# Optimization experiments

Measured on AMD Instinct MI355X. Metric: run time of the kernel, lower is better.

The kernel has to match this reference:

```python
import jax, jax.numpy as jnp
import numpy as np

DIM = 768
D_STATE = 64
D_CONV = 4
EXPAND = 2
D_INNER = EXPAND * DIM          # 1536
DT_RANK = (DIM + 15) // 16      # 48
BATCH = 2
SEQ = 1024
EPS = 1e-5


def setup_inputs() -> dict:
    key = jax.random.key(0)
    ks = jax.random.split(key, 10)
    s = 0.02
    x = jax.random.normal(ks[0], (BATCH, SEQ, DIM), dtype=jnp.float32)
    gamma = jnp.ones((DIM,), jnp.float32)
    beta = jnp.zeros((DIM,), jnp.float32)
    W_in = jax.random.normal(ks[1], (2 * D_INNER, DIM), jnp.float32) * s
    conv_w = jax.random.normal(ks[2], (D_INNER, D_CONV), jnp.float32) * s
    conv_b = jnp.zeros((D_INNER,), jnp.float32)
    W_x = jax.random.normal(ks[3], (DT_RANK + 2 * D_STATE, D_INNER), jnp.float32) * s
    W_dt = jax.random.normal(ks[4], (D_INNER, DT_RANK), jnp.float32) * s
    b_dt = jax.random.uniform(ks[5], (D_INNER,), jnp.float32, -4.0, -2.0)  # dt bias ~ log-space init
    # S4D-real init: A_log[d, n] = log(n+1)
    A_log = jnp.log(jnp.broadcast_to(jnp.arange(1, D_STATE + 1, dtype=jnp.float32), (D_INNER, D_STATE)))
    D = jnp.ones((D_INNER,), jnp.float32)
    W_out = jax.random.normal(ks[6], (DIM, D_INNER), jnp.float32) * s
    return {"x": x, "gamma": gamma, "beta": beta, "W_in": W_in,
            "conv_w": conv_w, "conv_b": conv_b, "W_x": W_x,
            "W_dt": W_dt, "b_dt": b_dt, "A_log": A_log, "D": D, "W_out": W_out}


def _silu(v):
    return v * jax.nn.sigmoid(v)


def _mamba_forward(x, gamma, beta, W_in, conv_w, conv_b, W_x, W_dt, b_dt, A_log, D, W_out):
    B, L, _ = x.shape
    # LayerNorm
    mu = jnp.mean(x, axis=-1, keepdims=True)
    var = jnp.mean(jnp.square(x - mu), axis=-1, keepdims=True)
    xn = (x - mu) * jax.lax.rsqrt(var + EPS) * gamma + beta
    # in_proj -> (u, z)
    xz = jnp.einsum('bld,ed->ble', xn, W_in)          # [B, L, 2*D_INNER]
    u, z = jnp.split(xz, 2, axis=-1)                  # each [B, L, D_INNER]
    # depthwise causal conv1d along L
    uc = jnp.transpose(u, (0, 2, 1))                  # [B, C, L]
    uc = jnp.pad(uc, ((0, 0), (0, 0), (D_CONV - 1, 0)))
    kern = conv_w[:, None, :]                         # [C, 1, K]
    uc = jax.lax.conv_general_dilated(
        uc, kern, window_strides=(1,), padding='VALID',
        feature_group_count=D_INNER,
        dimension_numbers=('NCH', 'OIH', 'NCH'))
    uc = uc + conv_b[None, :, None]
    u = _silu(jnp.transpose(uc, (0, 2, 1)))           # [B, L, D_INNER]
    # x_proj -> (dt, Bssm, Cssm)
    x_dbl = jnp.einsum('blc,ec->ble', u, W_x)
    dt = x_dbl[..., :DT_RANK]
    Bssm = x_dbl[..., DT_RANK:DT_RANK + D_STATE]      # [B, L, N]
    Cssm = x_dbl[..., DT_RANK + D_STATE:]             # [B, L, N]
    delta = jax.nn.softplus(jnp.einsum('blr,cr->blc', dt, W_dt) + b_dt)  # [B, L, C]
    A = -jnp.exp(A_log)                               # [C, N]

    # selective scan, time-major
    d_t = jnp.transpose(delta, (1, 0, 2))             # [L, B, C]
    B_t = jnp.transpose(Bssm, (1, 0, 2))              # [L, B, N]
    C_t = jnp.transpose(Cssm, (1, 0, 2))              # [L, B, N]
    u_t = jnp.transpose(u, (1, 0, 2))                 # [L, B, C]

    def step(h, inp):
        d, b, c, uu = inp
        dA = jnp.exp(d[..., None] * A)                # [B, C, N]
        h = dA * h + d[..., None] * b[:, None, :] * uu[..., None]
        y = jnp.sum(h * c[:, None, :], axis=-1) + D * uu
        return h, y

    h0 = jnp.zeros((B, D_INNER, D_STATE), x.dtype)
    _, ys = jax.lax.scan(step, h0, (d_t, B_t, C_t, u_t))
    y = jnp.transpose(ys, (1, 0, 2))                  # [B, L, C]
    y = y * _silu(z)
    return jnp.einsum('blc,dc->bld', y, W_out)


def reference(x, gamma, beta, W_in, conv_w, conv_b, W_x, W_dt, b_dt, A_log, D, W_out):
    return _mamba_forward(x, gamma, beta, W_in, conv_w, conv_b, W_x,
                          W_dt, b_dt, A_log, D, W_out)
```

## Files before the change

kernel.cpp:

```cpp
#include <hip/hip_runtime.h>
#include <math.h>

#define DIMD 768
#define DSTATE 64
#define DINNER 1536
#define DTRANK 48
#define BATCH 2
#define SEQL 1024
#define NTOK (BATCH*SEQL)
#define XDBL_P 192
#define EPSV 1e-5f

typedef __attribute__((ext_vector_type(8))) short bf16x8;
typedef __attribute__((ext_vector_type(4))) float f32x4;

__device__ inline short f2bf(float f) {
  unsigned u = __float_as_uint(f);
  u = u + 0x7FFFu + ((u >> 16) & 1u);
  return (short)(u >> 16);
}

__global__ __launch_bounds__(256) void ln_kernel(const float* __restrict__ x,
                                                 const float* __restrict__ gamma,
                                                 const float* __restrict__ beta,
                                                 short* __restrict__ xnq) {
  int wave = threadIdx.x >> 6;
  int lane = threadIdx.x & 63;
  int row = blockIdx.x * 4 + wave;
  if (row >= NTOK) return;
  const float* xr = x + (size_t)row * DIMD;
  float v[12];
  float s = 0.f, ss = 0.f;
#pragma unroll
  for (int i = 0; i < 12; ++i) {
    v[i] = xr[lane + i*64];
    s += v[i];
    ss += v[i]*v[i];
  }
#pragma unroll
  for (int m = 1; m < 64; m <<= 1) {
    s  += __shfl_xor(s, m);
    ss += __shfl_xor(ss, m);
  }
  float mu   = s * (1.f/DIMD);
  float var  = ss * (1.f/DIMD) - mu*mu;
  float rstd = rsqrtf(var + EPSV);
  short* o = xnq + (size_t)row * DIMD;
#pragma unroll
  for (int i = 0; i < 12; ++i) {
    int j = lane + i*64;
    o[j] = f2bf((v[i] - mu) * rstd * gamma[j] + beta[j]);
  }
}

#define NW_IN  (3072*768)
#define NW_OUT (768*1536)
#define NW_XP  (192*1536)
__global__ __launch_bounds__(256) void cvt_weights_kernel(const float* __restrict__ Win,
                                                          const float* __restrict__ Wout,
                                                          const float* __restrict__ Wx,
                                                          short* __restrict__ qin,
                                                          short* __restrict__ qout,
                                                          short* __restrict__ qx) {
  int idx = blockIdx.x * 256 + threadIdx.x;
  if (idx < NW_IN) { qin[idx] = f2bf(Win[idx]); return; }
  idx -= NW_IN;
  if (idx < NW_OUT) { qout[idx] = f2bf(Wout[idx]); return; }
  idx -= NW_OUT;
  if (idx < NW_XP) {
    int r = idx / 1536;
    qx[idx] = (r < 176) ? f2bf(Wx[idx]) : (short)0;
  }
}

template<int BN>
__global__ __launch_bounds__(256) void gemm_mfma(const short* __restrict__ A,
                                                 const short* __restrict__ B,
                                                 float* __restrict__ C, int ldc,
                                                 int Kfull, int Kchunk, size_t partStride) {
  constexpr int BM = 128, BK = 64;
  constexpr int WN = (BN == 128) ? 2 : 1;
  constexpr int WM = 4 / WN;
  constexpr int MFR = BM / (WM * 16);
  constexpr int NFR = BN / (WN * 16);
  constexpr int BSW = (BN * BK * 2) / 4096;
  __shared__ short As[BM * BK];
  __shared__ short Bs[BN * BK];
  const int tid  = threadIdx.x;
  const int wave = tid >> 6, lane = tid & 63;
  const int m0 = blockIdx.y * BM;
  const int n0 = blockIdx.x * BN;
  const int wm = wave / WN, wn = wave % WN;
  const int kBeg = blockIdx.z * Kchunk;
  const int kEnd = kBeg + Kchunk;
  C += (size_t)blockIdx.z * partStride;

  const short* aSrc = A + (size_t)(m0 + (tid >> 3)) * Kfull + (tid & 7) * 8;
  const short* bSrc = B + (size_t)(n0 + (tid >> 3)) * Kfull + (tid & 7) * 8;

  f32x4 acc[MFR][NFR];
#pragma unroll
  for (int i = 0; i < MFR; ++i)
#pragma unroll
    for (int j = 0; j < NFR; ++j)
      acc[i][j] = (f32x4){0.f, 0.f, 0.f, 0.f};

  for (int k0 = kBeg; k0 < kEnd; k0 += BK) {
#pragma unroll
    for (int s = 0; s < 4; ++s)
      __builtin_amdgcn_global_load_lds(
        (const __attribute__((address_space(1))) void*)(aSrc + (size_t)s*32*Kfull + k0),
        (__attribute__((address_space(3))) void*)((char*)As + s*4096 + wave*1024),
        16, 0, 0);
#pragma unroll
    for (int s = 0; s < BSW; ++s)
      __builtin_amdgcn_global_load_lds(
        (const __attribute__((address_space(1))) void*)(bSrc + (size_t)s*32*Kfull + k0),
        (__attribute__((address_space(3))) void*)((char*)Bs + s*4096 + wave*1024),
        16, 0, 0);
    __syncthreads();

#pragma unroll
    for (int kk = 0; kk < 2; ++kk) {
      bf16x8 af[MFR], bfr[NFR];
#pragma unroll
      for (int i = 0; i < MFR; ++i) {
        int r = wm * (BM / WM) + i * 16 + (lane & 15);
        af[i] = *(const bf16x8*)&As[r * BK + kk * 32 + (lane >> 4) * 8];
      }
#pragma unroll
      for (int j = 0; j < NFR; ++j) {
        int r = wn * (BN / WN) + j * 16 + (lane & 15);
        bfr[j] = *(const bf16x8*)&Bs[r * BK + kk * 32 + (lane >> 4) * 8];
      }
#pragma unroll
      for (int i = 0; i < MFR; ++i)
#pragma unroll
        for (int j = 0; j < NFR; ++j)
          acc[i][j] = __builtin_amdgcn_mfma_f32_16x16x32_bf16(af[i], bfr[j], acc[i][j], 0, 0, 0);
    }
    __syncthreads();
  }

  const int cn = lane & 15, cr4 = (lane >> 4) * 4;
#pragma unroll
  for (int i = 0; i < MFR; ++i)
#pragma unroll
    for (int j = 0; j < NFR; ++j)
#pragma unroll
      for (int r = 0; r < 4; ++r) {
        int m = m0 + wm * (BM / WM) + i * 16 + cr4 + r;
        int n = n0 + wn * (BN / WN) + j * 16 + cn;
        C[(size_t)m * ldc + n] = acc[i][j][r];
      }
}

__global__ __launch_bounds__(256) void reduce4_kernel(const float* __restrict__ p,
                                                      float* __restrict__ outb) {
  const int n4 = NTOK * XDBL_P / 4;
  int i = blockIdx.x * 256 + threadIdx.x;
  if (i >= n4) return;
  const float4* p4 = (const float4*)p;
  float4 a = p4[i];
  float4 b = p4[i + n4];
  float4 c = p4[i + 2*n4];
  float4 d = p4[i + 3*n4];
  float4 r;
  r.x = ((a.x + b.x) + c.x) + d.x;
  r.y = ((a.y + b.y) + c.y) + d.y;
  r.z = ((a.z + b.z) + c.z) + d.z;
  r.w = ((a.w + b.w) + c.w) + d.w;
  ((float4*)outb)[i] = r;
}

template<int ACT>
__global__ __launch_bounds__(256) void gemm_nt(const float* __restrict__ A, int lda,
                                               const float* __restrict__ W, int ldw,
                                               const float* __restrict__ bias,
                                               float* __restrict__ C, int ldc,
                                               int M, int N, int K) {
  __shared__ float Asl[16][68];
  __shared__ float Wsl[16][68];
  int tid = threadIdx.x;
  int m0 = blockIdx.y * 64;
  int n0 = blockIdx.x * 64;
  int lrow = tid >> 2;
  int lq   = tid & 3;
  int tx = tid & 15;
  int ty = tid >> 4;
  float acc[4][4] = {{0.f}};

  for (int k0 = 0; k0 < K; k0 += 16) {
    float4 av = make_float4(0.f,0.f,0.f,0.f);
    int ar = m0 + lrow;
    if (ar < M) av = *(const float4*)(A + (size_t)ar*lda + k0 + lq*4);
    float4 wv = make_float4(0.f,0.f,0.f,0.f);
    int wr = n0 + lrow;
    if (wr < N) wv = *(const float4*)(W + (size_t)wr*ldw + k0 + lq*4);
    __syncthreads();
    Asl[lq*4+0][lrow] = av.x; Asl[lq*4+1][lrow] = av.y;
    Asl[lq*4+2][lrow] = av.z; Asl[lq*4+3][lrow] = av.w;
    Wsl[lq*4+0][lrow] = wv.x; Wsl[lq*4+1][lrow] = wv.y;
    Wsl[lq*4+2][lrow] = wv.z; Wsl[lq*4+3][lrow] = wv.w;
    __syncthreads();
#pragma unroll
    for (int kk = 0; kk < 16; ++kk) {
      float4 a4 = *(const float4*)&Asl[kk][ty*4];
      float4 w4 = *(const float4*)&Wsl[kk][tx*4];
      float a[4] = {a4.x, a4.y, a4.z, a4.w};
      float w[4] = {w4.x, w4.y, w4.z, w4.w};
#pragma unroll
      for (int i = 0; i < 4; ++i)
#pragma unroll
        for (int j = 0; j < 4; ++j)
          acc[i][j] += a[i]*w[j];
    }
  }

#pragma unroll
  for (int i = 0; i < 4; ++i) {
    int m = m0 + ty*4 + i;
    if (m >= M) continue;
    float* crow = C + (size_t)m*ldc;
    float bm = (ACT == 2) ? bias[m] : 0.f;
#pragma unroll
    for (int j = 0; j < 4; ++j) {
      int n = n0 + tx*4 + j;
      if (n >= N) continue;
      float val = acc[i][j];
      if (ACT == 2) {
        val += bm;
        val = (val > 20.f) ? val : log1pf(__expf(val));
      }
      crow[n] = val;
    }
  }
}

__global__ __launch_bounds__(256) void conv_silu_kernel(const float* __restrict__ xz,
                                                        const float* __restrict__ conv_w,
                                                        const float* __restrict__ conv_b,
                                                        float* __restrict__ uT,
                                                        short* __restrict__ ucq) {
  __shared__ float tile[64][65];
  int b  = blockIdx.z;
  int c0 = blockIdx.x * 64;
  int t0 = blockIdx.y * 64;
  int lx = threadIdx.x & 63;
  int ly = threadIdx.x >> 6;
  int c = c0 + lx;
  const int S = 2*DINNER;
  float w0 = conv_w[c*4+0], w1 = conv_w[c*4+1], w2 = conv_w[c*4+2], w3 = conv_w[c*4+3];
  float cb = conv_b[c];
  int ts = t0 + ly*16;
  const float* col = xz + ((size_t)b*SEQL + ts) * S + c;
  float x3 = (ts >= 3) ? col[-3*S] : 0.f;
  float x2 = (ts >= 2) ? col[-2*S] : 0.f;
  float x1 = (ts >= 1) ? col[-1*S] : 0.f;
#pragma unroll
  for (int i = 0; i < 16; ++i) {
    float x0 = col[(size_t)i*S];
    float acc = cb + x3*w0 + x2*w1 + x1*w2 + x0*w3;
    float sig = 1.f / (1.f + __expf(-acc));
    float v = acc * sig;
    ucq[((size_t)b*SEQL + ts + i)*DINNER + c] = f2bf(v);
    tile[lx][ly*16 + i] = v;
    x3 = x2; x2 = x1; x1 = x0;
  }
  __syncthreads();
#pragma unroll
  for (int i = 0; i < 16; ++i) {
    int cl = ly*16 + i;
    uT[((size_t)(c0 + cl))*NTOK + (size_t)b*SEQL + t0 + lx] = tile[cl][lx];
  }
}

__device__ inline float readlane_f(float v, int l) {
  return __int_as_float(__builtin_amdgcn_readlane(__float_as_int(v), l));
}

__global__ __launch_bounds__(256) void scan_kernel(const float* __restrict__ dT,
                                                   const float* __restrict__ x_dbl,
                                                   const float* __restrict__ uT,
                                                   const float* __restrict__ A_log,
                                                   const float* __restrict__ Dp,
                                                   float* __restrict__ yT) {
  __shared__ float red_all[4][32*66 + 32];
  int tid  = threadIdx.x;
  int wave = tid >> 6;
  int lane = tid & 63;
  float* red = red_all[wave];
  int ch = blockIdx.x * 4 + wave;
  int b = ch / DINNER;
  int c = ch % DINNER;
  float Ac2 = -__expf(A_log[(size_t)c*64 + lane]) * 1.44269504f;
  float Dc = Dp[c];
  float h = 0.f;
  const float* dp = dT + (size_t)c * NTOK + (size_t)b * SEQL;
  const float* up = uT + (size_t)c * NTOK + (size_t)b * SEQL;
  float* yrow = yT + ((size_t)b*DINNER + c) * SEQL;
  const float* xB = x_dbl + ((size_t)b * SEQL) * XDBL_P + DTRANK + lane;

  float d_v = dp[lane];
  float u_v = up[lane];

  const int r = lane & 31, hs = lane >> 5;
  const int NBLK = SEQL/64;
  for (int tb = 0; tb < NBLK; ++tb) {
    int t0 = tb*64;
    float d_nxt = 0.f, u_nxt = 0.f;
    if (tb + 1 < NBLK) {
      d_nxt = dp[t0 + 64 + lane];
      u_nxt = up[t0 + 64 + lane];
    }
    float du_v = d_v * u_v;

#pragma unroll
    for (int half = 0; half < 2; ++half) {
      const float* xh = xB + (size_t)(t0 + half*32) * XDBL_P;
#pragma unroll
      for (int k = 0; k < 32; ++k) {
        int i = half*32 + k;
        float Bv = xh[(size_t)k * XDBL_P];
        float Cv = xh[(size_t)k * XDBL_P + DSTATE];
        float sd  = readlane_f(d_v,  i);
        float sdu = readlane_f(du_v, i);
        float dA = __builtin_amdgcn_exp2f(sd * Ac2);
        h = fmaf(dA, h, sdu * Bv);
        red[k*66 + lane] = h * Cv;
      }
      {
        const float2* rp2 = (const float2*)&red[r*66 + hs*32];
        float2 a0 = rp2[0], a1 = rp2[1];
#pragma unroll
        for (int jj = 1; jj < 8; ++jj) {
          float2 v0 = rp2[2*jj], v1 = rp2[2*jj + 1];
          a0.x += v0.x; a0.y += v0.y;
          a1.x += v1.x; a1.y += v1.y;
        }
        float y = (a0.x + a0.y) + (a1.x + a1.y);
        y += __shfl_xor(y, 32);
        float ut = __shfl(u_v, half*32 + r);
        y = fmaf(Dc, ut, y);
        if (lane < 32) yrow[t0 + half*32 + lane] = y;
      }
    }
    __syncthreads();
    d_v = d_nxt;
    u_v = u_nxt;
  }
}

__global__ __launch_bounds__(256) void ymul_kernel(const float* __restrict__ yT,
                                                   const float* __restrict__ xz,
                                                   short* __restrict__ g) {
  __shared__ float tile[64][65];
  int b  = blockIdx.z;
  int c0 = blockIdx.x * 64;
  int t0 = blockIdx.y * 64;
  int lx = threadIdx.x & 63;
  int ly = threadIdx.x >> 6;
  const float* src = yT + ((size_t)b*DINNER + c0) * SEQL + t0;
#pragma unroll
  for (int i = 0; i < 16; ++i) {
    int c = ly*16 + i;
    tile[c][lx] = src[(size_t)c*SEQL + lx];
  }
  __syncthreads();
  const int S = 2*DINNER;
#pragma unroll
  for (int i = 0; i < 16; ++i) {
    int t = ly*16 + i;
    float z = xz[((size_t)b*SEQL + t0 + t)*S + DINNER + c0 + lx];
    float zs = z / (1.f + __expf(-z));
    g[((size_t)b*SEQL + t0 + t)*DINNER + c0 + lx] = f2bf(tile[lx][t] * zs);
  }
}

extern "C" void kernel_launch(void* const* d_in, const int* in_sizes, int n_in,
                              void* d_out, int out_size, void* d_ws, size_t ws_size,
                              hipStream_t stream) {
  const float* x      = (const float*)d_in[0];
  const float* gamma  = (const float*)d_in[1];
  const float* beta   = (const float*)d_in[2];
  const float* W_in   = (const float*)d_in[3];
  const float* conv_w = (const float*)d_in[4];
  const float* conv_b = (const float*)d_in[5];
  const float* W_x    = (const float*)d_in[6];
  const float* W_dt   = (const float*)d_in[7];
  const float* b_dt   = (const float*)d_in[8];
  const float* A_log  = (const float*)d_in[9];
  const float* Dvec   = (const float*)d_in[10];
  const float* W_out  = (const float*)d_in[11];
  float* out = (float*)d_out;

  float* ws = (float*)d_ws;
  float* xz    = ws;
  float* uT    = xz    + (size_t)NTOK*3072;
  float* xdbl  = uT    + (size_t)NTOK*1536;
  float* dltT  = xdbl  + (size_t)NTOK*XDBL_P;
  float* yT    = dltT  + (size_t)NTOK*1536;
  float* xpart = yT    + (size_t)NTOK*1536;
  short* xnq   = (short*)(xpart + (size_t)4*NTOK*XDBL_P);
  short* ucq   = xnq  + (size_t)NTOK*768;
  short* gq    = ucq  + (size_t)NTOK*1536;
  short* qin   = gq   + (size_t)NTOK*1536;
  short* qx    = qin  + (size_t)NW_IN;
  short* qout  = qx   + (size_t)NW_XP;

  cvt_weights_kernel<<<(NW_IN+NW_OUT+NW_XP+255)/256, 256, 0, stream>>>(W_in, W_out, W_x, qin, qout, qx);
  ln_kernel<<<NTOK/4, 256, 0, stream>>>(x, gamma, beta, xnq);
  gemm_mfma<64><<<dim3(3072/64, NTOK/128), 256, 0, stream>>>(xnq, qin, xz, 3072, DIMD, DIMD, 0);
  conv_silu_kernel<<<dim3(DINNER/64, SEQL/64, BATCH), 256, 0, stream>>>(xz, conv_w, conv_b, uT, ucq);
  gemm_mfma<64><<<dim3(XDBL_P/64, NTOK/128, 4), 256, 0, stream>>>(ucq, qx, xpart, XDBL_P,
                                                                  DINNER, DINNER/4,
                                                                  (size_t)NTOK*XDBL_P);
  reduce4_kernel<<<(NTOK*XDBL_P/4 + 255)/256, 256, 0, stream>>>(xpart, xdbl);
  gemm_nt<2><<<dim3(NTOK/64, DINNER/64), 256, 0, stream>>>(W_dt, DTRANK, xdbl, XDBL_P, b_dt,
                                                           dltT, NTOK, DINNER, NTOK, DTRANK);
  scan_kernel<<<BATCH*DINNER/4, 256, 0, stream>>>(dltT, xdbl, uT, A_log, Dvec, yT);
  ymul_kernel<<<dim3(DINNER/64, SEQL/64, BATCH), 256, 0, stream>>>(yT, xz, gq);
  gemm_mfma<64><<<dim3(DIMD/64, NTOK/128), 256, 0, stream>>>(gq, qout, out, DIMD, DINNER, DINNER, 0);
}
```

Before: 184.5 us.

## Store in_proj output as bf16, merge LN and weight conversion kernels

The in_proj GEMM now writes its xz result as bf16 instead of fp32, and the conv and gating kernels read bf16. This halves that intermediate's write and read traffic. LayerNorm and weight conversion are merged into one prep launch to save a kernel launch. Scan indexing is also reworked to a running offset. The cost is extra rounding of u and z to bf16, which loses some precision.

Result: faster. 180.6 us (-2.1%).

```diff
diff --git a/kernel.cpp b/kernel.cpp
--- a/kernel.cpp
+++ b/kernel.cpp
@@ -19,50 +19,54 @@
   u = u + 0x7FFFu + ((u >> 16) & 1u);
   return (short)(u >> 16);
 }
-
-__global__ __launch_bounds__(256) void ln_kernel(const float* __restrict__ x,
-                                                 const float* __restrict__ gamma,
-                                                 const float* __restrict__ beta,
-                                                 short* __restrict__ xnq) {
-  int wave = threadIdx.x >> 6;
-  int lane = threadIdx.x & 63;
-  int row = blockIdx.x * 4 + wave;
-  if (row >= NTOK) return;
-  const float* xr = x + (size_t)row * DIMD;
-  float v[12];
-  float s = 0.f, ss = 0.f;
-#pragma unroll
-  for (int i = 0; i < 12; ++i) {
-    v[i] = xr[lane + i*64];
-    s += v[i];
-    ss += v[i]*v[i];
-  }
-#pragma unroll
-  for (int m = 1; m < 64; m <<= 1) {
-    s  += __shfl_xor(s, m);
-    ss += __shfl_xor(ss, m);
-  }
-  float mu   = s * (1.f/DIMD);
-  float var  = ss * (1.f/DIMD) - mu*mu;
-  float rstd = rsqrtf(var + EPSV);
-  short* o = xnq + (size_t)row * DIMD;
-#pragma unroll
-  for (int i = 0; i < 12; ++i) {
-    int j = lane + i*64;
-    o[j] = f2bf((v[i] - mu) * rstd * gamma[j] + beta[j]);
-  }
+__device__ inline float bf2f(short s) {
+  return __uint_as_float(((unsigned)(unsigned short)s) << 16);
 }
 
 #define NW_IN  (3072*768)
 #define NW_OUT (768*1536)
 #define NW_XP  (192*1536)
-__global__ __launch_bounds__(256) void cvt_weights_kernel(const float* __restrict__ Win,
-                                                          const float* __restrict__ Wout,
-                                                          const float* __restrict__ Wx,
-                                                          short* __restrict__ qin,
-                                                          short* __restrict__ qout,
-                                                          short* __restrict__ qx) {
-  int idx = blockIdx.x * 256 + threadIdx.x;
+#define LN_BLOCKS (NTOK/4)
+__global__ __launch_bounds__(256) void prep_kernel(const float* __restrict__ x,
+                                                   const float* __restrict__ gamma,
+                                                   const float* __restrict__ beta,
+                                                   short* __restrict__ xnq,
+                                                   const float* __restrict__ Win,
+                                                   const float* __restrict__ Wout,
+                                                   const float* __restrict__ Wx,
+                                                   short* __restrict__ qin,
+                                                   short* __restrict__ qout,
+                                                   short* __restrict__ qx) {
+  if (blockIdx.x < LN_BLOCKS) {
+    int wave = threadIdx.x >> 6;
+    int lane = threadIdx.x & 63;
+    int row = blockIdx.x * 4 + wave;
+    const float* xr = x + (size_t)row * DIMD;
+    float v[12];
+    float s = 0.f, ss = 0.f;
+#pragma unroll
+    for (int i = 0; i < 12; ++i) {
+      v[i] = xr[lane + i*64];
+      s += v[i];
+      ss += v[i]*v[i];
+    }
+#pragma unroll
+    for (int m = 1; m < 64; m <<= 1) {
+      s  += __shfl_xor(s, m);
+      ss += __shfl_xor(ss, m);
+    }
+    float mu   = s * (1.f/DIMD);
+    float var  = ss * (1.f/DIMD) - mu*mu;
+    float rstd = rsqrtf(var + EPSV);
+    short* o = xnq + (size_t)row * DIMD;
+#pragma unroll
+    for (int i = 0; i < 12; ++i) {
+      int j = lane + i*64;
+      o[j] = f2bf((v[i] - mu) * rstd * gamma[j] + beta[j]);
+    }
+    return;
+  }
+  int idx = (blockIdx.x - LN_BLOCKS) * 256 + threadIdx.x;
   if (idx < NW_IN) { qin[idx] = f2bf(Win[idx]); return; }
   idx -= NW_IN;
   if (idx < NW_OUT) { qout[idx] = f2bf(Wout[idx]); return; }
@@ -73,7 +77,7 @@
   }
 }
 
-template<int BN>
+template<int BN, bool BF16OUT>
 __global__ __launch_bounds__(256) void gemm_mfma(const short* __restrict__ A,
                                                  const short* __restrict__ B,
                                                  float* __restrict__ C, int ldc,
@@ -151,7 +155,10 @@
       for (int r = 0; r < 4; ++r) {
         int m = m0 + wm * (BM / WM) + i * 16 + cr4 + r;
         int n = n0 + wn * (BN / WN) + j * 16 + cn;
-        C[(size_t)m * ldc + n] = acc[i][j][r];
+        if constexpr (BF16OUT)
+          ((short*)C)[(size_t)m * ldc + n] = f2bf(acc[i][j][r]);
+        else
+          C[(size_t)m * ldc + n] = acc[i][j][r];
       }
 }
 
@@ -237,7 +244,7 @@
   }
 }
 
-__global__ __launch_bounds__(256) void conv_silu_kernel(const float* __restrict__ xz,
+__global__ __launch_bounds__(256) void conv_silu_kernel(const short* __restrict__ xzq,
                                                         const float* __restrict__ conv_w,
                                                         const float* __restrict__ conv_b,
                                                         float* __restrict__ uT,
@@ -253,13 +260,13 @@
   float w0 = conv_w[c*4+0], w1 = conv_w[c*4+1], w2 = conv_w[c*4+2], w3 = conv_w[c*4+3];
   float cb = conv_b[c];
   int ts = t0 + ly*16;
-  const float* col = xz + ((size_t)b*SEQL + ts) * S + c;
-  float x3 = (ts >= 3) ? col[-3*S] : 0.f;
-  float x2 = (ts >= 2) ? col[-2*S] : 0.f;
-  float x1 = (ts >= 1) ? col[-1*S] : 0.f;
+  const short* col = xzq + ((size_t)b*SEQL + ts) * S + c;
+  float x3 = (ts >= 3) ? bf2f(col[-3*S]) : 0.f;
+  float x2 = (ts >= 2) ? bf2f(col[-2*S]) : 0.f;
+  float x1 = (ts >= 1) ? bf2f(col[-1*S]) : 0.f;
 #pragma unroll
   for (int i = 0; i < 16; ++i) {
-    float x0 = col[(size_t)i*S];
+    float x0 = bf2f(col[(size_t)i*S]);
     float acc = cb + x3*w0 + x2*w1 + x1*w2 + x0*w3;
     float sig = 1.f / (1.f + __expf(-acc));
     float v = acc * sig;
@@ -279,6 +286,7 @@
   return __int_as_float(__builtin_amdgcn_readlane(__float_as_int(v), l));
 }
 
+#define CPB (DINNER/4)
 __global__ __launch_bounds__(256) void scan_kernel(const float* __restrict__ dT,
                                                    const float* __restrict__ x_dbl,
                                                    const float* __restrict__ uT,
@@ -290,19 +298,19 @@
   int wave = tid >> 6;
   int lane = tid & 63;
   float* red = red_all[wave];
-  int ch = blockIdx.x * 4 + wave;
-  int b = ch / DINNER;
-  int c = ch % DINNER;
+  int b = blockIdx.x / CPB;
+  int c = (blockIdx.x % CPB) * 4 + wave;
   float Ac2 = -__expf(A_log[(size_t)c*64 + lane]) * 1.44269504f;
   float Dc = Dp[c];
   float h = 0.f;
   const float* dp = dT + (size_t)c * NTOK + (size_t)b * SEQL;
   const float* up = uT + (size_t)c * NTOK + (size_t)b * SEQL;
   float* yrow = yT + ((size_t)b*DINNER + c) * SEQL;
-  const float* xB = x_dbl + ((size_t)b * SEQL) * XDBL_P + DTRANK + lane;
+  const float* sbase = x_dbl + (size_t)b * SEQL * XDBL_P + DTRANK;
 
   float d_v = dp[lane];
   float u_v = up[lane];
+  int off = lane;
 
   const int r = lane & 31, hs = lane >> 5;
   const int NBLK = SEQL/64;
@@ -317,12 +325,12 @@
 
 #pragma unroll
     for (int half = 0; half < 2; ++half) {
-      const float* xh = xB + (size_t)(t0 + half*32) * XDBL_P;
 #pragma unroll
       for (int k = 0; k < 32; ++k) {
         int i = half*32 + k;
-        float Bv = xh[(size_t)k * XDBL_P];
-        float Cv = xh[(size_t)k * XDBL_P + DSTATE];
+        float Bv = sbase[off];
+        float Cv = sbase[off + DSTATE];
+        off += XDBL_P;
         float sd  = readlane_f(d_v,  i);
         float sdu = readlane_f(du_v, i);
         float dA = __builtin_amdgcn_exp2f(sd * Ac2);
@@ -352,7 +360,7 @@
 }
 
 __global__ __launch_bounds__(256) void ymul_kernel(const float* __restrict__ yT,
-                                                   const float* __restrict__ xz,
+                                                   const short* __restrict__ xzq,
                                                    short* __restrict__ g) {
   __shared__ float tile[64][65];
   int b  = blockIdx.z;
@@ -371,7 +379,7 @@
 #pragma unroll
   for (int i = 0; i < 16; ++i) {
     int t = ly*16 + i;
-    float z = xz[((size_t)b*SEQL + t0 + t)*S + DINNER + c0 + lx];
+    float z = bf2f(xzq[((size_t)b*SEQL + t0 + t)*S + DINNER + c0 + lx]);
     float zs = z / (1.f + __expf(-z));
     g[((size_t)b*SEQL + t0 + t)*DINNER + c0 + lx] = f2bf(tile[lx][t] * zs);
   }
@@ -395,30 +403,32 @@
   float* out = (float*)d_out;
 
   float* ws = (float*)d_ws;
-  float* xz    = ws;
-  float* uT    = xz    + (size_t)NTOK*3072;
+  float* uT    = ws;
   float* xdbl  = uT    + (size_t)NTOK*1536;
   float* dltT  = xdbl  + (size_t)NTOK*XDBL_P;
   float* yT    = dltT  + (size_t)NTOK*1536;
   float* xpart = yT    + (size_t)NTOK*1536;
-  short* xnq   = (short*)(xpart + (size_t)4*NTOK*XDBL_P);
+  short* xzq   = (short*)(xpart + (size_t)4*NTOK*XDBL_P);
+  short* xnq   = xzq  + (size_t)NTOK*3072;
   short* ucq   = xnq  + (size_t)NTOK*768;
   short* gq    = ucq  + (size_t)NTOK*1536;
   short* qin   = gq   + (size_t)NTOK*1536;
   short* qx    = qin  + (size_t)NW_IN;
   short* qout  = qx   + (size_t)NW_XP;
 
-  cvt_weights_kernel<<<(NW_IN+NW_OUT+NW_XP+255)/256, 256, 0, stream>>>(W_in, W_out, W_x, qin, qout, qx);
-  ln_kernel<<<NTOK/4, 256, 0, stream>>>(x, gamma, beta, xnq);
-  gemm_mfma<64><<<dim3(3072/64, NTOK/128), 256, 0, stream>>>(xnq, qin, xz, 3072, DIMD, DIMD, 0);
-  conv_silu_kernel<<<dim3(DINNER/64, SEQL/64, BATCH), 256, 0, stream>>>(xz, conv_w, conv_b, uT, ucq);
-  gemm_mfma<64><<<dim3(XDBL_P/64, NTOK/128, 4), 256, 0, stream>>>(ucq, qx, xpart, XDBL_P,
-                                                                  DINNER, DINNER/4,
-                                                                  (size_t)NTOK*XDBL_P);
+  prep_kernel<<<LN_BLOCKS + (NW_IN+NW_OUT+NW_XP+255)/256, 256, 0, stream>>>(
+      x, gamma, beta, xnq, W_in, W_out, W_x, qin, qout, qx);
+  gemm_mfma<64,true><<<dim3(3072/64, NTOK/128), 256, 0, stream>>>(
+      xnq, qin, (float*)xzq, 3072, DIMD, DIMD, 0);
+  conv_silu_kernel<<<dim3(DINNER/64, SEQL/64, BATCH), 256, 0, stream>>>(
+      xzq, conv_w, conv_b, uT, ucq);
+  gemm_mfma<64,false><<<dim3(XDBL_P/64, NTOK/128, 4), 256, 0, stream>>>(
+      ucq, qx, xpart, XDBL_P, DINNER, DINNER/4, (size_t)NTOK*XDBL_P);
   reduce4_kernel<<<(NTOK*XDBL_P/4 + 255)/256, 256, 0, stream>>>(xpart, xdbl);
   gemm_nt<2><<<dim3(NTOK/64, DINNER/64), 256, 0, stream>>>(W_dt, DTRANK, xdbl, XDBL_P, b_dt,
                                                            dltT, NTOK, DINNER, NTOK, DTRANK);
   scan_kernel<<<BATCH*DINNER/4, 256, 0, stream>>>(dltT, xdbl, uT, A_log, Dvec, yT);
-  ymul_kernel<<<dim3(DINNER/64, SEQL/64, BATCH), 256, 0, stream>>>(yT, xz, gq);
-  gemm_mfma<64><<<dim3(DIMD/64, NTOK/128), 256, 0, stream>>>(gq, qout, out, DIMD, DINNER, DINNER, 0);
-}
+  ymul_kernel<<<dim3(DINNER/64, SEQL/64, BATCH), 256, 0, stream>>>(yT, xzq, gq);
+  gemm_mfma<64,false><<<dim3(DIMD/64, NTOK/128), 256, 0, stream>>>(
+      gq, qout, out, DIMD, DINNER, DINNER, 0);
+}
```
